# Optimization experiments

Measured on AMD Instinct MI355X. Metric: run time of the kernel, lower is better.

Reference implementation:

```python
import jax, jax.numpy as jnp
import numpy as np

DIM = 1024
HEADS = 16
DIM_HEAD = 64
INNER = HEADS * DIM_HEAD
EPS = 1e-5


def layernorm(x, g, b):
    mu = jnp.mean(x, axis=-1, keepdims=True)
    var = jnp.mean((x - mu) ** 2, axis=-1, keepdims=True)
    return (x - mu) * jax.lax.rsqrt(var + EPS) * g + b


def setup_inputs() -> dict:
    key = jax.random.key(0)
    ks = jax.random.split(key, 8)
    B, S = 2, 2048
    s_in = (2.0 / DIM) ** 0.5
    return {
        "x": jax.random.normal(ks[0], (B, S, DIM), jnp.float32),
        "w_qkv": jax.random.normal(ks[1], (DIM, 3 * INNER), jnp.float32) * s_in,
        "w_out": jax.random.normal(ks[2], (INNER, DIM), jnp.float32) * s_in,
        "b_out": jnp.zeros((DIM,), jnp.float32),
        "g1": jnp.ones((DIM,), jnp.float32),
        "beta1": jnp.zeros((DIM,), jnp.float32),
        "g2": jnp.ones((DIM,), jnp.float32),
        "beta2": jnp.zeros((DIM,), jnp.float32),
        "w_ff1": jax.random.normal(ks[3], (DIM, 4 * DIM), jnp.float32) * s_in,
        "b_ff1": jnp.zeros((4 * DIM,), jnp.float32),
        "w_ff2": jax.random.normal(ks[4], (4 * DIM, DIM), jnp.float32) * (2.0 / (4 * DIM)) ** 0.5,
        "b_ff2": jnp.zeros((DIM,), jnp.float32),
    }


def reference(x, w_qkv, w_out, b_out, g1, beta1, g2, beta2, w_ff1, b_ff1, w_ff2, b_ff2):
    B, S, D = x.shape
    scale = DIM_HEAD ** -0.5
    # --- attention block (pre-norm) ---
    h = layernorm(x, g1, beta1)
    qkv = h @ w_qkv  # [B,S,3*INNER]
    q, k, v = jnp.split(qkv, 3, axis=-1)
    def heads(t):
        return t.reshape(B, S, HEADS, DIM_HEAD).transpose(0, 2, 1, 3)  # [B,H,S,dh]
    q, k, v = heads(q), heads(k), heads(v)
    attn = jnp.einsum("bhsd,bhtd->bhst", q, k) * scale
    attn = jax.nn.softmax(attn, axis=-1)
    out = jnp.einsum("bhst,bhtd->bhsd", attn, v)
    out = out.transpose(0, 2, 1, 3).reshape(B, S, INNER)
    x = x + out @ w_out + b_out
    # --- FFN block (pre-norm) ---
    h = layernorm(x, g2, beta2)
    h = jax.nn.gelu(h @ w_ff1 + b_ff1, approximate=False)
    x = x + h @ w_ff2 + b_ff2
    return x
```

## Files before the change

kernel.cpp:

```cpp
#include <hip/hip_runtime.h>
#include <math.h>

typedef unsigned short u16;
typedef __attribute__((ext_vector_type(4))) float f32x4;
typedef __attribute__((ext_vector_type(16))) float f32x16;
typedef __attribute__((ext_vector_type(4))) unsigned short u16x4;
typedef __attribute__((ext_vector_type(8))) __bf16 bf16x8;

static constexpr int SS   = 2048;
static constexpr int DD   = 1024;
static constexpr int HH   = 16;
static constexpr int DH   = 64;
static constexpr int NTOK = 4096;
static constexpr int NQKV = 3072;

#define DEV static __device__ __forceinline__
#define GLD_AS1(p) ((__attribute__((address_space(1))) void*)(void*)(p))
#define GLD_AS3(p) ((__attribute__((address_space(3))) void*)(p))

#define WAIT_BAR(N) asm volatile("s_waitcnt vmcnt(" #N ")\n\ts_barrier" ::: "memory")
#define BAR()       asm volatile("s_barrier" ::: "memory")

DEV u16 f2bf(float f) {
    union { float f; unsigned int i; } v; v.f = f;
    unsigned int r = v.i + 0x7fffu + ((v.i >> 16) & 1u);
    return (u16)(r >> 16);
}
DEV float bdec(u16 u) {
    union { unsigned int i; float f; } v; v.i = ((unsigned int)u) << 16; return v.f;
}

DEV f32x4 MFMA(bf16x8 a, bf16x8 b, f32x4 c) {
    return __builtin_amdgcn_mfma_f32_16x16x32_bf16(a, b, c, 0, 0, 0);
}
DEV f32x16 MFMA32(bf16x8 a, bf16x8 b, f32x16 c) {
    return __builtin_amdgcn_mfma_f32_32x32x16_bf16(a, b, c, 0, 0, 0);
}
DEV f32x16 zero16() {
    f32x16 z;
    #pragma unroll
    for (int i = 0; i < 16; i++) z[i] = 0.f;
    return z;
}

__global__ __launch_bounds__(256)
void k_transpose(const float* __restrict__ in, u16* __restrict__ out, int R, int C) {
    __shared__ float tile[32][33];
    int c0 = blockIdx.x * 32, r0 = blockIdx.y * 32;
    int tx = threadIdx.x, ty = threadIdx.y;
    #pragma unroll
    for (int i = 0; i < 32; i += 8)
        tile[ty + i][tx] = in[(size_t)(r0 + ty + i) * C + c0 + tx];
    __syncthreads();
    #pragma unroll
    for (int i = 0; i < 32; i += 8)
        out[(size_t)(c0 + ty + i) * R + r0 + tx] = f2bf(tile[tx][ty + i]);
}

__global__ __launch_bounds__(256)
void k_layernorm(const float* __restrict__ x, const float* __restrict__ g,
                 const float* __restrict__ b, u16* __restrict__ out) {
    int row = blockIdx.x, t = threadIdx.x;
    const float4* xp = reinterpret_cast<const float4*>(x + (size_t)row * DD);
    float4 v = xp[t];
    float s = v.x + v.y + v.z + v.w;
    float q = v.x * v.x + v.y * v.y + v.z * v.z + v.w * v.w;
    #pragma unroll
    for (int m = 1; m < 64; m <<= 1) { s += __shfl_xor(s, m); q += __shfl_xor(q, m); }
    __shared__ float ps[4], pq[4];
    int w = t >> 6, l = t & 63;
    if (l == 0) { ps[w] = s; pq[w] = q; }
    __syncthreads();
    s = ps[0] + ps[1] + ps[2] + ps[3];
    q = pq[0] + pq[1] + pq[2] + pq[3];
    float mu = s * (1.0f / DD);
    float var = q * (1.0f / DD) - mu * mu;
    float rstd = rsqrtf(var + 1e-5f);
    float4 gv = reinterpret_cast<const float4*>(g)[t];
    float4 bv = reinterpret_cast<const float4*>(b)[t];
    u16x4 o;
    o.x = f2bf((v.x - mu) * rstd * gv.x + bv.x);
    o.y = f2bf((v.y - mu) * rstd * gv.y + bv.y);
    o.z = f2bf((v.z - mu) * rstd * gv.z + bv.z);
    o.w = f2bf((v.w - mu) * rstd * gv.w + bv.w);
    reinterpret_cast<u16x4*>(out + (size_t)row * DD)[t] = o;
}

template<int MODE>
__global__ __launch_bounds__(256)
void k_gemm(const u16* __restrict__ A, const u16* __restrict__ BT,
            float* __restrict__ Cf, u16* __restrict__ Cb,
            const float* __restrict__ bias, const float* __restrict__ res,
            u16* __restrict__ vT, int M, int N, int K) {
    __shared__ __align__(128) char lds[2][32768];
    const int t = threadIdx.x;
    const int w = t >> 6, l = t & 63;
    const int lg = l >> 4, lr = l & 15;
    const int m0 = blockIdx.y * 128, n0 = blockIdx.x * 128;
    const int wr = w >> 1, wc = w & 1;

    int kbeg = 0, kend = K;
    if (MODE == 3) {
        const int kh = K >> 1;
        kbeg = blockIdx.z * kh;
        kend = kbeg + kh;
    }

    const int csw = ((l & 7) ^ (l >> 3)) << 3;
    const int chunk0 = w * 4;
    const int srow = (l >> 3);

    f32x4 acc[4][4];
    #pragma unroll
    for (int i = 0; i < 4; i++)
        #pragma unroll
        for (int j = 0; j < 4; j++)
            acc[i][j] = (f32x4){0.f, 0.f, 0.f, 0.f};

    #pragma unroll
    for (int i = 0; i < 4; i++) {
        const int chunk = chunk0 + i;
        const int r = chunk * 8 + srow;
        __builtin_amdgcn_global_load_lds(GLD_AS1(A  + (size_t)(m0 + r) * K + kbeg + csw),
                                         GLD_AS3(lds[0] + chunk * 1024), 16, 0, 0);
        __builtin_amdgcn_global_load_lds(GLD_AS1(BT + (size_t)(n0 + r) * K + kbeg + csw),
                                         GLD_AS3(lds[0] + 16384 + chunk * 1024), 16, 0, 0);
    }

    int buf = 0;
    for (int kt = kbeg; kt < kend; kt += 64) {
        if (kt + 64 < kend) {
            #pragma unroll
            for (int i = 0; i < 4; i++) {
                const int chunk = chunk0 + i;
                const int r = chunk * 8 + srow;
                __builtin_amdgcn_global_load_lds(GLD_AS1(A  + (size_t)(m0 + r) * K + kt + 64 + csw),
                                                 GLD_AS3(lds[buf ^ 1] + chunk * 1024), 16, 0, 0);
                __builtin_amdgcn_global_load_lds(GLD_AS1(BT + (size_t)(n0 + r) * K + kt + 64 + csw),
                                                 GLD_AS3(lds[buf ^ 1] + 16384 + chunk * 1024), 16, 0, 0);
            }
            WAIT_BAR(8);
        } else {
            WAIT_BAR(0);
        }
        const char* Al = lds[buf];
        const char* Bl = lds[buf] + 16384;
        #pragma unroll
        for (int s = 0; s < 2; s++) {
            const int swz = (s * 64 + lg * 16) ^ ((lr & 7) << 4);
            bf16x8 af[4], bfr[4];
            #pragma unroll
            for (int mi = 0; mi < 4; mi++)
                af[mi] = *reinterpret_cast<const bf16x8*>(Al + (wr * 64 + mi * 16 + lr) * 128 + swz);
            #pragma unroll
            for (int ni = 0; ni < 4; ni++)
                bfr[ni] = *reinterpret_cast<const bf16x8*>(Bl + (wc * 64 + ni * 16 + lr) * 128 + swz);
            #pragma unroll
            for (int mi = 0; mi < 4; mi++)
                #pragma unroll
                for (int ni = 0; ni < 4; ni++)
                    acc[mi][ni] = MFMA(af[mi], bfr[ni], acc[mi][ni]);
        }
        BAR();
        buf ^= 1;
    }

    #pragma unroll
    for (int mi = 0; mi < 4; mi++) {
        #pragma unroll
        for (int ni = 0; ni < 4; ni++) {
            int nn = n0 + wc * 64 + ni * 16 + lr;
            #pragma unroll
            for (int r = 0; r < 4; r++) {
                int mm = m0 + wr * 64 + mi * 16 + lg * 4 + r;
                float v = acc[mi][ni][r];
                if (MODE == 0) {
                    if (nn < 2048) {
                        float sv = (nn < 1024) ? v * 0.18033688011112042f : v;
                        Cb[(size_t)mm * NQKV + nn] = f2bf(sv);
                    } else {
                        int b = mm >> 11, sIdx = mm & 2047;
                        int hd = nn - 2048;
                        vT[(((size_t)(b * HH + (hd >> 6)) * DH) + (hd & 63)) * SS + sIdx] = f2bf(v);
                    }
                } else if (MODE == 2) {
                    float u = v + bias[nn];
                    float gl = 0.5f * u * (1.0f + erff(u * 0.70710678118654752f));
                    Cb[(size_t)mm * N + nn] = f2bf(gl);
                } else {
                    u16* dst = blockIdx.z ? vT : Cb;
                    dst[(size_t)mm * N + nn] = f2bf(v);
                }
            }
        }
    }
}

__global__ __launch_bounds__(256)
void k_ffreduce(const float* __restrict__ RES, const u16* __restrict__ P0,
                const u16* __restrict__ P1, const float* __restrict__ bias,
                float* __restrict__ OUT) {
    int i = blockIdx.x * 256 + threadIdx.x;
    float4 xv = reinterpret_cast<const float4*>(RES)[i];
    u16x4 a = reinterpret_cast<const u16x4*>(P0)[i];
    u16x4 b = reinterpret_cast<const u16x4*>(P1)[i];
    float4 bv = reinterpret_cast<const float4*>(bias)[i & (DD / 4 - 1)];
    float4 o;
    o.x = xv.x + bdec(a.x) + bdec(b.x) + bv.x;
    o.y = xv.y + bdec(a.y) + bdec(b.y) + bv.y;
    o.z = xv.z + bdec(a.z) + bdec(b.z) + bv.z;
    o.w = xv.w + bdec(a.w) + bdec(b.w) + bv.w;
    reinterpret_cast<float4*>(OUT)[i] = o;
}

__global__ __launch_bounds__(256)
void k_attn(const u16* __restrict__ qkv, const u16* __restrict__ vT,
            u16* __restrict__ out) {
    const int w = threadIdx.x >> 6, l = threadIdx.x & 63;
    const int q = l & 31, hi = l >> 5;
    const int task = (blockIdx.x & 7) * 64 + (blockIdx.x >> 3);
    const int bh = task >> 4;
    const int qg = task & 15;
    const int b = bh >> 4, h = bh & 15;
    const size_t rowbase = (size_t)b * SS;
    const int q0 = (qg * 4 + w) * 32;

    __shared__ __align__(128) u16 Kl[2][64 * 64];
    __shared__ __align__(128) u16 Vl[2][64 * 64];

    const u16* kbase = qkv + rowbase * NQKV + 1024 + h * DH;
    const u16* vbase = vT + (size_t)bh * DH * SS;

    const int srow8 = l >> 3;
    const int sslot = (l & 7) ^ srow8;
    const int kr0 = w * 8 + srow8;
    const u16* kg0 = kbase + (size_t)kr0 * NQKV + sslot * 8;
    const u16* kg1 = kbase + (size_t)(kr0 + 32) * NQKV + sslot * 8;
    const u16* vg0 = vbase + (size_t)kr0 * SS + sslot * 8;
    const u16* vg1 = vbase + (size_t)(kr0 + 32) * SS + sslot * 8;
    const int chA = (w * 8) * 64, chB = (w * 8 + 32) * 64;

    const u16* qrow = qkv + (rowbase + q0 + q) * NQKV + h * DH + hi * 8;
    bf16x8 qf[4];
    #pragma unroll
    for (int ks = 0; ks < 4; ks++)
        qf[ks] = *reinterpret_cast<const bf16x8*>(qrow + ks * 16);
    asm volatile("s_waitcnt vmcnt(0)" ::: "memory");

    bf16x8 onesf;
    #pragma unroll
    for (int i = 0; i < 8; i++) onesf[i] = (__bf16)1.0f;

    f32x16 o0 = zero16(), o1 = zero16();
    f32x16 lacc = zero16();

    __builtin_amdgcn_global_load_lds(GLD_AS1(kg0), GLD_AS3((u16*)Kl[0] + chA), 16, 0, 0);
    __builtin_amdgcn_global_load_lds(GLD_AS1(kg1), GLD_AS3((u16*)Kl[0] + chB), 16, 0, 0);
    __builtin_amdgcn_global_load_lds(GLD_AS1(vg0), GLD_AS3((u16*)Vl[0] + chA), 16, 0, 0);
    __builtin_amdgcn_global_load_lds(GLD_AS1(vg1), GLD_AS3((u16*)Vl[0] + chB), 16, 0, 0);

    int buf = 0;
    for (int kv0 = 0; kv0 < SS; kv0 += 64) {
        if (kv0 + 64 < SS) {
            __builtin_amdgcn_global_load_lds(GLD_AS1(kg0 + (size_t)(kv0 + 64) * NQKV),
                                             GLD_AS3((u16*)Kl[buf ^ 1] + chA), 16, 0, 0);
            __builtin_amdgcn_global_load_lds(GLD_AS1(kg1 + (size_t)(kv0 + 64) * NQKV),
                                             GLD_AS3((u16*)Kl[buf ^ 1] + chB), 16, 0, 0);
            __builtin_amdgcn_global_load_lds(GLD_AS1(vg0 + (kv0 + 64)),
                                             GLD_AS3((u16*)Vl[buf ^ 1] + chA), 16, 0, 0);
            __builtin_amdgcn_global_load_lds(GLD_AS1(vg1 + (kv0 + 64)),
                                             GLD_AS3((u16*)Vl[buf ^ 1] + chB), 16, 0, 0);
            WAIT_BAR(4);
        } else {
            WAIT_BAR(0);
        }
        const u16* Kb = Kl[buf];
        const u16* Vb = Vl[buf];
        const int qsw = (q & 7) << 3;

        f32x16 st0 = zero16(), st1 = zero16();
        #pragma unroll
        for (int ks = 0; ks < 4; ks++) {
            const int off = (ks * 16 + hi * 8) ^ qsw;
            bf16x8 kf0 = *reinterpret_cast<const bf16x8*>(Kb + q * 64 + off);
            bf16x8 kf1 = *reinterpret_cast<const bf16x8*>(Kb + (q + 32) * 64 + off);
            st0 = MFMA32(kf0, qf[ks], st0);
            st1 = MFMA32(kf1, qf[ks], st1);
        }

        f32x16 p0, p1;
        #pragma unroll
        for (int i = 0; i < 16; i++) p0[i] = exp2f(st0[i]);
        #pragma unroll
        for (int i = 0; i < 16; i++) p1[i] = exp2f(st1[i]);

        union W { unsigned int u; __bf16 h[2]; };
        W pw[16];
        #pragma unroll
        for (int m = 0; m < 8; m++) {
            pw[m].h[0] = (__bf16)p0[2 * m];
            pw[m].h[1] = (__bf16)p0[2 * m + 1];
            pw[8 + m].h[0] = (__bf16)p1[2 * m];
            pw[8 + m].h[1] = (__bf16)p1[2 * m + 1];
        }

        bf16x8 pf[4];
        #pragma unroll
        for (int kk = 0; kk < 4; kk++) {
            const int base = (kk >> 1) * 8 + (kk & 1) * 4;
            unsigned int a0 = pw[base + 0].u, a1 = pw[base + 1].u;
            unsigned int b0 = pw[base + 2].u, b1 = pw[base + 3].u;
            unsigned int own0 = hi ? b0 : a0, own1 = hi ? b1 : a1;
            unsigned int snd0 = hi ? a0 : b0, snd1 = hi ? a1 : b1;
            unsigned int r0 = __shfl_xor(snd0, 32), r1 = __shfl_xor(snd1, 32);
            union F { unsigned int u[4]; bf16x8 v; } f;
            f.u[0] = hi ? r0 : own0;
            f.u[1] = hi ? r1 : own1;
            f.u[2] = hi ? own0 : r0;
            f.u[3] = hi ? own1 : r1;
            pf[kk] = f.v;
        }

        #pragma unroll
        for (int kk = 0; kk < 4; kk++) {
            const int off = (kk * 16 + hi * 8) ^ qsw;
            bf16x8 v0 = *reinterpret_cast<const bf16x8*>(Vb + q * 64 + off);
            bf16x8 v1 = *reinterpret_cast<const bf16x8*>(Vb + (q + 32) * 64 + off);
            lacc = MFMA32(onesf, pf[kk], lacc);
            o0 = MFMA32(v0, pf[kk], o0);
            o1 = MFMA32(v1, pf[kk], o1);
        }

        BAR();
        buf ^= 1;
    }

    float invl = 1.0f / lacc[0];
    u16* orow = out + (rowbase + q0 + q) * DD + h * DH + hi * 4;
    #pragma unroll
    for (int a = 0; a < 4; a++) {
        u16x4 s0v, s1v;
        #pragma unroll
        for (int i = 0; i < 4; i++) {
            s0v[i] = f2bf(o0[4 * a + i] * invl);
            s1v[i] = f2bf(o1[4 * a + i] * invl);
        }
        *reinterpret_cast<u16x4*>(orow + 8 * a)      = s0v;
        *reinterpret_cast<u16x4*>(orow + 32 + 8 * a) = s1v;
    }
}

extern "C" void kernel_launch(void* const* d_in, const int* in_sizes, int n_in,
                              void* d_out, int out_size, void* d_ws, size_t ws_size,
                              hipStream_t stream) {
    (void)in_sizes; (void)n_in; (void)out_size; (void)ws_size;
    const float* x     = (const float*)d_in[0];
    const float* w_qkv = (const float*)d_in[1];
    const float* w_out = (const float*)d_in[2];
    const float* b_out = (const float*)d_in[3];
    const float* g1    = (const float*)d_in[4];
    const float* be1   = (const float*)d_in[5];
    const float* g2    = (const float*)d_in[6];
    const float* be2   = (const float*)d_in[7];
    const float* w_ff1 = (const float*)d_in[8];
    const float* b_ff1 = (const float*)d_in[9];
    const float* w_ff2 = (const float*)d_in[10];
    const float* b_ff2 = (const float*)d_in[11];

    char* ws = (char*)d_ws;
    u16*   W  = (u16*)(ws);
    u16*   Hb = (u16*)(ws + 8388608);
    u16*   QF = (u16*)(ws + 16777216);
    u16*   VT = (u16*)(ws + 50331648);
    u16*   AO = (u16*)(ws + 58720256);
    float* X1 = (float*)(ws + 67108864);
    float* OUT = (float*)d_out;

    k_layernorm<<<NTOK, 256, 0, stream>>>(x, g1, be1, Hb);
    k_transpose<<<dim3(3072 / 32, 1024 / 32), dim3(32, 8), 0, stream>>>(w_qkv, W, 1024, 3072);
    k_gemm<0><<<dim3(3072 / 128, 4096 / 128), 256, 0, stream>>>(
        Hb, W, nullptr, QF, nullptr, nullptr, VT, NTOK, NQKV, 1024);
    k_attn<<<512, 256, 0, stream>>>(QF, VT, AO);
    k_transpose<<<dim3(1024 / 32, 1024 / 32), dim3(32, 8), 0, stream>>>(w_out, W, 1024, 1024);
    k_gemm<3><<<dim3(1024 / 128, 4096 / 128, 2), 256, 0, stream>>>(
        AO, W, nullptr, Hb, nullptr, nullptr, VT, NTOK, 1024, 1024);
    k_ffreduce<<<NTOK * DD / 4 / 256, 256, 0, stream>>>(x, Hb, VT, b_out, X1);
    k_layernorm<<<NTOK, 256, 0, stream>>>(X1, g2, be2, Hb);
    k_transpose<<<dim3(4096 / 32, 1024 / 32), dim3(32, 8), 0, stream>>>(w_ff1, W, 1024, 4096);
    k_gemm<2><<<dim3(4096 / 128, 4096 / 128), 256, 0, stream>>>(
        Hb, W, nullptr, QF, b_ff1, nullptr, nullptr, NTOK, 4096, 1024);
    k_transpose<<<dim3(1024 / 32, 4096 / 32), dim3(32, 8), 0, stream>>>(w_ff2, W, 4096, 1024);
    k_gemm<3><<<dim3(1024 / 128, 4096 / 128, 2), 256, 0, stream>>>(
        QF, W, nullptr, VT, nullptr, nullptr, AO, NTOK, 1024, 4096);
    k_ffreduce<<<NTOK * DD / 4 / 256, 256, 0, stream>>>(X1, VT, AO, b_ff2, OUT);
}
```

Measured before the change: 292.5 us.

## Split V transpose out of QKV epilogue, fuse reduce+layernorm, approximate GELU

The QKV GEMM epilogue now writes V row-major like Q and K, and a new LDS-tiled kernel transposes V into the per-head layout, replacing scattered strided stores. The attention residual reduction and the second layernorm are fused into one kernel, which avoids re-reading X1. The erf-based GELU in the FF1 epilogue is replaced by a tanh-style approximation computed with exp2, trading exactness for cheaper math. The extra transpose launch adds a pass over V.

```diff
diff --git a/kernel.cpp b/kernel.cpp
--- a/kernel.cpp
+++ b/kernel.cpp
@@ -55,6 +55,27 @@
     #pragma unroll
     for (int i = 0; i < 32; i += 8)
         out[(size_t)(c0 + ty + i) * R + r0 + tx] = f2bf(tile[tx][ty + i]);
+}
+
+__global__ __launch_bounds__(256)
+void k_transpose_v(const u16* __restrict__ qkv, u16* __restrict__ vT) {
+    __shared__ u16 tile[32][33];
+    int bid = blockIdx.x;
+    int st = bid & 63;
+    int dt = (bid >> 6) & 1;
+    int bh = bid >> 7;
+    int b = bh >> 4, h = bh & 15;
+    int s0 = st * 32, d0 = dt * 32;
+    int tx = threadIdx.x & 31, ty = threadIdx.x >> 5;
+    const u16* src = qkv + ((size_t)(b * SS + s0)) * NQKV + 2048 + h * DH + d0;
+    #pragma unroll
+    for (int i = 0; i < 32; i += 8)
+        tile[ty + i][tx] = src[(size_t)(ty + i) * NQKV + tx];
+    __syncthreads();
+    u16* dst = vT + ((size_t)bh * DH + d0) * SS + s0;
+    #pragma unroll
+    for (int i = 0; i < 32; i += 8)
+        dst[(size_t)(ty + i) * SS + tx] = tile[tx][ty + i];
 }
 
 __global__ __launch_bounds__(256)
@@ -86,6 +107,46 @@
     reinterpret_cast<u16x4*>(out + (size_t)row * DD)[t] = o;
 }
 
+__global__ __launch_bounds__(256)
+void k_redln(const float* __restrict__ x, const u16* __restrict__ P0,
+             const u16* __restrict__ P1, const float* __restrict__ bias,
+             const float* __restrict__ g, const float* __restrict__ be,
+             float* __restrict__ X1, u16* __restrict__ LNout) {
+    int row = blockIdx.x, t = threadIdx.x;
+    size_t i = (size_t)row * 256 + t;
+    float4 xv = reinterpret_cast<const float4*>(x)[i];
+    u16x4 a = reinterpret_cast<const u16x4*>(P0)[i];
+    u16x4 bb = reinterpret_cast<const u16x4*>(P1)[i];
+    float4 bv = reinterpret_cast<const float4*>(bias)[t];
+    float4 v;
+    v.x = xv.x + bdec(a.x) + bdec(bb.x) + bv.x;
+    v.y = xv.y + bdec(a.y) + bdec(bb.y) + bv.y;
+    v.z = xv.z + bdec(a.z) + bdec(bb.z) + bv.z;
+    v.w = xv.w + bdec(a.w) + bdec(bb.w) + bv.w;
+    reinterpret_cast<float4*>(X1)[i] = v;
+    float s = v.x + v.y + v.z + v.w;
+    float q = v.x * v.x + v.y * v.y + v.z * v.z + v.w * v.w;
+    #pragma unroll
+    for (int m = 1; m < 64; m <<= 1) { s += __shfl_xor(s, m); q += __shfl_xor(q, m); }
+    __shared__ float ps[4], pq[4];
+    int w = t >> 6, l = t & 63;
+    if (l == 0) { ps[w] = s; pq[w] = q; }
+    __syncthreads();
+    s = ps[0] + ps[1] + ps[2] + ps[3];
+    q = pq[0] + pq[1] + pq[2] + pq[3];
+    float mu = s * (1.0f / DD);
+    float var = q * (1.0f / DD) - mu * mu;
+    float rstd = rsqrtf(var + 1e-5f);
+    float4 gv = reinterpret_cast<const float4*>(g)[t];
+    float4 ev = reinterpret_cast<const float4*>(be)[t];
+    u16x4 o;
+    o.x = f2bf((v.x - mu) * rstd * gv.x + ev.x);
+    o.y = f2bf((v.y - mu) * rstd * gv.y + ev.y);
+    o.z = f2bf((v.z - mu) * rstd * gv.z + ev.z);
+    o.w = f2bf((v.w - mu) * rstd * gv.w + ev.w);
+    reinterpret_cast<u16x4*>(LNout + (size_t)row * DD)[t] = o;
+}
+
 template<int MODE>
 __global__ __launch_bounds__(256)
 void k_gemm(const u16* __restrict__ A, const u16* __restrict__ BT,
@@ -175,17 +236,12 @@
                 int mm = m0 + wr * 64 + mi * 16 + lg * 4 + r;
                 float v = acc[mi][ni][r];
                 if (MODE == 0) {
-                    if (nn < 2048) {
-                        float sv = (nn < 1024) ? v * 0.18033688011112042f : v;
-                        Cb[(size_t)mm * NQKV + nn] = f2bf(sv);
-                    } else {
-                        int b = mm >> 11, sIdx = mm & 2047;
-                        int hd = nn - 2048;
-                        vT[(((size_t)(b * HH + (hd >> 6)) * DH) + (hd & 63)) * SS + sIdx] = f2bf(v);
-                    }
+                    float sv = (nn < 1024) ? v * 0.18033688011112042f : v;
+                    Cb[(size_t)mm * NQKV + nn] = f2bf(sv);
                 } else if (MODE == 2) {
                     float u = v + bias[nn];
-                    float gl = 0.5f * u * (1.0f + erff(u * 0.70710678118654752f));
+                    float u3 = u * u * u;
+                    float gl = u / (1.0f + exp2f(-2.3022077f * u - 0.10294276f * u3));
                     Cb[(size_t)mm * N + nn] = f2bf(gl);
                 } else {
                     u16* dst = blockIdx.z ? vT : Cb;
@@ -379,18 +435,18 @@
     k_layernorm<<<NTOK, 256, 0, stream>>>(x, g1, be1, Hb);
     k_transpose<<<dim3(3072 / 32, 1024 / 32), dim3(32, 8), 0, stream>>>(w_qkv, W, 1024, 3072);
     k_gemm<0><<<dim3(3072 / 128, 4096 / 128), 256, 0, stream>>>(
-        Hb, W, nullptr, QF, nullptr, nullptr, VT, NTOK, NQKV, 1024);
+        Hb, W, nullptr, QF, nullptr, nullptr, nullptr, NTOK, NQKV, 1024);
+    k_transpose_v<<<4096, 256, 0, stream>>>(QF, VT);
     k_attn<<<512, 256, 0, stream>>>(QF, VT, AO);
     k_transpose<<<dim3(1024 / 32, 1024 / 32), dim3(32, 8), 0, stream>>>(w_out, W, 1024, 1024);
     k_gemm<3><<<dim3(1024 / 128, 4096 / 128, 2), 256, 0, stream>>>(
         AO, W, nullptr, Hb, nullptr, nullptr, VT, NTOK, 1024, 1024);
-    k_ffreduce<<<NTOK * DD / 4 / 256, 256, 0, stream>>>(x, Hb, VT, b_out, X1);
-    k_layernorm<<<NTOK, 256, 0, stream>>>(X1, g2, be2, Hb);
+    k_redln<<<NTOK, 256, 0, stream>>>(x, Hb, VT, b_out, g2, be2, X1, AO);
     k_transpose<<<dim3(4096 / 32, 1024 / 32), dim3(32, 8), 0, stream>>>(w_ff1, W, 1024, 4096);
     k_gemm<2><<<dim3(4096 / 128, 4096 / 128), 256, 0, stream>>>(
-        Hb, W, nullptr, QF, b_ff1, nullptr, nullptr, NTOK, 4096, 1024);
+        AO, W, nullptr, QF, b_ff1, nullptr, nullptr, NTOK, 4096, 1024);
     k_transpose<<<dim3(1024 / 32, 4096 / 32), dim3(32, 8), 0, stream>>>(w_ff2, W, 4096, 1024);
     k_gemm<3><<<dim3(1024 / 128, 4096 / 128, 2), 256, 0, stream>>>(
-        QF, W, nullptr, VT, nullptr, nullptr, AO, NTOK, 1024, 4096);
-    k_ffreduce<<<NTOK * DD / 4 / 256, 256, 0, stream>>>(X1, VT, AO, b_ff2, OUT);
-}
+        QF, W, nullptr, VT, nullptr, nullptr, Hb, NTOK, 1024, 4096);
+    k_ffreduce<<<NTOK * DD / 4 / 256, 256, 0, stream>>>(X1, VT, Hb, b_ff2, OUT);
+}
```

Measured after the change: 266.0 us. 1.1x faster.
